# Optimization experiments

Hardware: AMD Instinct MI355X
Metric: run time of the kernel (lower is better)

The kernel has to match this reference:

```python
import jax, jax.numpy as jnp
import numpy as np

C = 19          # EEG channels
NP = C * C      # 361 channel pairs
D = 256         # UNIFIED_FEATURE_DIM
H = 8           # num_heads
HD = D // H     # head dim


def _build_mask():
    # rel[p, q] = True iff key-pair q shares a channel with query-pair p
    idx = np.arange(NP)
    ci, cj = idx // C, idx % C
    rel = ((ci[:, None] == ci[None, :]) | (ci[:, None] == cj[None, :]) |
           (cj[:, None] == ci[None, :]) | (cj[:, None] == cj[None, :]))
    return jnp.asarray(rel.reshape(C, C, NP))  # (channel_i, j, key_pair)

MASK = _build_mask()


def setup_inputs() -> dict:
    key = jax.random.key(0)
    ks = jax.random.split(key, 6)
    s = 0.05
    return {
        "x": jax.random.normal(ks[0], (32, NP, D), jnp.float32),
        # 19 stacked nn.MultiheadAttention modules: in_proj (3D, D) = [Wq; Wk; Wv]
        "w_in": jax.random.normal(ks[1], (C, 3 * D, D), jnp.float32) * s,
        "b_in": jnp.zeros((C, 3 * D), jnp.float32),
        "w_out": jax.random.normal(ks[2], (C, D, D), jnp.float32) * s,
        "b_out": jnp.zeros((C, D), jnp.float32),
        # fusion: nn.Linear(D, D)
        "w_fuse": jax.random.normal(ks[3], (D, D), jnp.float32) * s,
        "b_fuse": jnp.zeros((D,), jnp.float32),
    }


def reference(x, w_in, b_in, w_out, b_out, w_fuse, b_fuse):
    # x: (B, 361, D). Pair p=(i,j) at index i*19+j uses attention module i,
    # query = x[:, p], keys/values = pairs sharing channel i or j (mask).
    B = x.shape[0]
    wq, wk, wv = w_in[:, :D], w_in[:, D:2 * D], w_in[:, 2 * D:]
    bq, bk, bv = b_in[:, :D], b_in[:, D:2 * D], b_in[:, 2 * D:]

    # Per-channel K/V projections over all 361 pairs: (C, B, NP, D)
    K = jnp.einsum('bnd,ced->cbne', x, wk) + bk[:, None, None, :]
    V = jnp.einsum('bnd,ced->cbne', x, wv) + bv[:, None, None, :]
    # Queries grouped by first channel i: x reshaped to (B, C, C, D)
    xq = x.reshape(B, C, C, D)
    Q = jnp.einsum('bcjd,ced->cbje', xq, wq) + bq[:, None, None, :]  # (C,B,C,D)

    Qh = Q.reshape(C, B, C, H, HD)
    Kh = K.reshape(C, B, NP, H, HD)
    Vh = V.reshape(C, B, NP, H, HD)

    scale = 1.0 / jnp.sqrt(jnp.asarray(HD, x.dtype))
    scores = jnp.einsum('cbqhe,cbkhe->cbhqk', Qh, Kh) * scale  # (C,B,H,C,NP)
    scores = jnp.where(MASK[:, None, None, :, :], scores, -jnp.inf)
    attn = jax.nn.softmax(scores, axis=-1)

    out = jnp.einsum('cbhqk,cbkhe->cbqhe', attn, Vh).reshape(C, B, C, D)
    out = jnp.einsum('cbqd,ced->cbqe', out, w_out) + b_out[:, None, None, :]
    out = out.transpose(1, 0, 2, 3).reshape(B, NP, D)  # back to (B, 361, D)

    # fusion ('linear') + residual
    return out @ w_fuse.T + b_fuse + x
```

## Files before the change

### kernel.cpp

```cpp
#include <hip/hip_runtime.h>

#define CC 19
#define NPOS 361
#define NPAD 384
#define DIM 256
#define TKEY 32
#define NTILES 12

#define LDS_BYTES 33792

using bf16x8 = __attribute__((ext_vector_type(8))) short;
using f16x4  = __attribute__((ext_vector_type(4))) _Float16;
using floatx4 = __attribute__((ext_vector_type(4))) float;
using uintx2 = __attribute__((ext_vector_type(2))) unsigned int;

__device__ __forceinline__ unsigned short f2bf(float f) {
  unsigned u = __builtin_bit_cast(unsigned, f);
  u += 0x7fffu + ((u >> 16) & 1u);
  return (unsigned short)(u >> 16);
}

__device__ __forceinline__ f16x4 pack4h(float a, float b, float c2, float d) {
  const auto h01 = __builtin_amdgcn_cvt_pkrtz(a, b);
  const auto h23 = __builtin_amdgcn_cvt_pkrtz(c2, d);
  uintx2 uv = {__builtin_bit_cast(unsigned, h01), __builtin_bit_cast(unsigned, h23)};
  return __builtin_bit_cast(f16x4, uv);
}

__global__ void conv_all_kernel(const float* __restrict__ x,
                                const float* __restrict__ w_in,
                                const float* __restrict__ w_out,
                                const float* __restrict__ w_fuse,
                                unsigned short* __restrict__ ws) {
  const int j = blockIdx.x * 256 + threadIdx.x;
  float4 v = make_float4(0.f, 0.f, 0.f, 0.f);
  unsigned short* dst;
  if (j < 786432) {
    const int row = j >> 6;
    const int off = (j & 63) << 2;
    const int b = row / NPAD;
    const int r = row - b * NPAD;
    if (r < NPOS) v = *(const float4*)&x[(b * NPOS + r) * DIM + off];
    dst = &ws[row * DIM + off];
  } else if (j < 1720320) {
    const int k = j - 786432;
    v = *(const float4*)&w_in[k << 2];
    dst = &ws[3145728 + (k << 2)];
  } else if (j < 2031616) {
    const int k = j - 1720320;
    v = *(const float4*)&w_out[k << 2];
    dst = &ws[6881280 + (k << 2)];
  } else {
    const int k = j - 2031616;
    v = *(const float4*)&w_fuse[k << 2];
    dst = &ws[8126464 + (k << 2)];
  }
  ushort4 o;
  o.x = f2bf(v.x); o.y = f2bf(v.y); o.z = f2bf(v.z); o.w = f2bf(v.w);
  *(ushort4*)dst = o;
}

__launch_bounds__(512, 2)
__global__ void cgca_kernel(const float* __restrict__ xf,
                            const float* __restrict__ b_in,
                            const float* __restrict__ b_out,
                            const float* __restrict__ b_fuse,
                            const unsigned short* __restrict__ xbf,
                            const unsigned short* __restrict__ wibf,
                            const unsigned short* __restrict__ wobf,
                            const unsigned short* __restrict__ wfbf,
                            float* __restrict__ out) {
  const int bid = blockIdx.x;
  const int xcd = bid & 7;
  const int slot = bid >> 3;
  int c, b;
  if (slot < 64) {
    c = ((slot >> 5) << 3) + xcd;
    b = slot & 31;
  } else {
    const int widx = ((slot - 64) << 3) + xcd;
    c = 16 + (widx >> 5);
    b = widx & 31;
  }

  const int tid = threadIdx.x;
  const int w = tid >> 6;
  const int lane = tid & 63;
  const int quad = lane >> 4;
  const int l16 = lane & 15;
  const int eh = w * 32;

  extern __shared__ char smem[];
  unsigned short* bufx0 = (unsigned short*)(smem);
  unsigned short* bufx1 = (unsigned short*)(smem + 16896);
  float* sL = (float*)(smem + 16896);

  const float scale = 0.17677669529663687f;
  const floatx4 fzero = {0.f, 0.f, 0.f, 0.f};

  f16x4 qf[2][2];
  {
    bf16x8 wq[2][8];
#pragma unroll
    for (int m4 = 0; m4 < 2; ++m4)
#pragma unroll
      for (int k = 0; k < 8; ++k)
        wq[m4][k] = *(const bf16x8*)&wibf[(c * 768 + eh + m4 * 16 + l16) * DIM + k * 32 + quad * 8];
    float bq[2][4];
#pragma unroll
    for (int m4 = 0; m4 < 2; ++m4) {
      const float4 bv4 = *(const float4*)&b_in[c * 768 + eh + m4 * 16 + quad * 4];
      bq[m4][0] = bv4.x; bq[m4][1] = bv4.y; bq[m4][2] = bv4.z; bq[m4][3] = bv4.w;
    }
#pragma unroll
    for (int mt = 0; mt < 2; ++mt) {
      const int xrow = b * NPAD + c * CC + mt * 16 + l16;
      bf16x8 xq[8];
#pragma unroll
      for (int k = 0; k < 8; ++k)
        xq[k] = *(const bf16x8*)&xbf[xrow * DIM + k * 32 + quad * 8];
#pragma unroll
      for (int m4 = 0; m4 < 2; ++m4) {
        floatx4 acc = fzero;
#pragma unroll
        for (int k = 0; k < 8; ++k)
          acc = __builtin_amdgcn_mfma_f32_16x16x32_bf16(wq[m4][k], xq[k], acc, 0, 0, 0);
        qf[mt][m4] = pack4h((acc[0] + bq[m4][0]) * scale, (acc[1] + bq[m4][1]) * scale,
                            (acc[2] + bq[m4][2]) * scale, (acc[3] + bq[m4][3]) * scale);
      }
    }
  }

  bf16x8 wk[2][8], wv[2][8];
#pragma unroll
  for (int m4 = 0; m4 < 2; ++m4)
#pragma unroll
    for (int k = 0; k < 8; ++k) {
      wk[m4][k] =
          *(const bf16x8*)&wibf[(c * 768 + 256 + eh + m4 * 16 + l16) * DIM + k * 32 + quad * 8];
      wv[m4][k] =
          *(const bf16x8*)&wibf[(c * 768 + 512 + eh + m4 * 16 + l16) * DIM + k * 32 + quad * 8];
    }
  float bk[2][4];
#pragma unroll
  for (int m4 = 0; m4 < 2; ++m4) {
    const float4 bv4 = *(const float4*)&b_in[c * 768 + 256 + eh + m4 * 16 + quad * 4];
    bk[m4][0] = bv4.x; bk[m4][1] = bv4.y; bk[m4][2] = bv4.z; bk[m4][3] = bv4.w;
  }
  float bV[2];
#pragma unroll
  for (int ne = 0; ne < 2; ++ne) bV[ne] = b_in[c * 768 + 512 + eh + ne * 16 + l16];

#pragma unroll
  for (int it = 0; it < 2; ++it) {
    const int cc2 = tid + it * 512;
    const int row = cc2 >> 5;
    const int col = (cc2 & 31) * 8;
    *(bf16x8*)&bufx0[row * 264 + col] = *(const bf16x8*)&xbf[(b * NPAD + row) * DIM + col];
  }

  floatx4 o_acc[2][2];
  float lsum[2] = {0.f, 0.f};
#pragma unroll
  for (int mt = 0; mt < 2; ++mt)
#pragma unroll
    for (int ne = 0; ne < 2; ++ne) o_acc[mt][ne] = fzero;

  __syncthreads();

  for (int t = 0; t < NTILES; ++t) {
    const int t0 = t * TKEY;
    unsigned short* bx  = (t & 1) ? bufx1 : bufx0;
    unsigned short* bxn = (t & 1) ? bufx0 : bufx1;

    if (t + 1 < NTILES) {
#pragma unroll
      for (int it = 0; it < 2; ++it) {
        const int cc2 = tid + it * 512;
        const int row = cc2 >> 5;
        const int col = (cc2 & 31) * 8;
        *(bf16x8*)&bxn[row * 264 + col] =
            *(const bf16x8*)&xbf[(b * NPAD + t0 + TKEY + row) * DIM + col];
      }
    }

    floatx4 aK[2][2], aV[2][2];
#pragma unroll
    for (int i = 0; i < 2; ++i)
#pragma unroll
      for (int j = 0; j < 2; ++j) { aK[i][j] = fzero; aV[i][j] = fzero; }
#pragma unroll
    for (int k = 0; k < 8; ++k) {
      bf16x8 xfr[2];
#pragma unroll
      for (int n4 = 0; n4 < 2; ++n4)
        xfr[n4] = *(const bf16x8*)&bx[(n4 * 16 + l16) * 264 + k * 32 + quad * 8];
#pragma unroll
      for (int m4 = 0; m4 < 2; ++m4)
#pragma unroll
        for (int n4 = 0; n4 < 2; ++n4) {
          aK[m4][n4] = __builtin_amdgcn_mfma_f32_16x16x32_bf16(wk[m4][k], xfr[n4], aK[m4][n4], 0, 0, 0);
          aV[n4][m4] = __builtin_amdgcn_mfma_f32_16x16x32_bf16(xfr[n4], wv[m4][k], aV[n4][m4], 0, 0, 0);
        }
    }
    __syncthreads();

    f16x4 kf[2][2];
    f16x4 vf[2][2];
#pragma unroll
    for (int kt = 0; kt < 2; ++kt)
#pragma unroll
      for (int ec = 0; ec < 2; ++ec) {
        kf[kt][ec] = pack4h(aK[ec][kt][0] + bk[ec][0], aK[ec][kt][1] + bk[ec][1],
                            aK[ec][kt][2] + bk[ec][2], aK[ec][kt][3] + bk[ec][3]);
        vf[kt][ec] = pack4h(aV[kt][ec][0] + bV[ec], aV[kt][ec][1] + bV[ec],
                            aV[kt][ec][2] + bV[ec], aV[kt][ec][3] + bV[ec]);
      }

#pragma unroll
    for (int mt = 0; mt < 2; ++mt) {
      const unsigned q = (unsigned)(mt * 16 + l16);
      f16x4 pf[2];
#pragma unroll
      for (int kt = 0; kt < 2; ++kt) {
        floatx4 s = __builtin_amdgcn_mfma_f32_16x16x16f16(kf[kt][0], qf[mt][0], fzero, 0, 0, 0);
        s = __builtin_amdgcn_mfma_f32_16x16x16f16(kf[kt][1], qf[mt][1], s, 0, 0, 0);
        const int kbase = t0 + kt * 16 + quad * 4;
        float p[4];
#pragma unroll
        for (int r = 0; r < 4; ++r) {
          const int kabs = kbase + r;
          const unsigned ki = ((unsigned)kabs * 110377u) >> 21;
          const unsigned kj = (unsigned)kabs - ki * 19u;
          const bool ok = (kabs < NPOS) &&
                          (ki == (unsigned)c || kj == (unsigned)c || ki == q || kj == q);
          p[r] = ok ? __expf(s[r]) : 0.f;
        }
        lsum[mt] += (p[0] + p[1]) + (p[2] + p[3]);
        pf[kt] = pack4h(p[0], p[1], p[2], p[3]);
      }
#pragma unroll
      for (int kt = 0; kt < 2; ++kt)
#pragma unroll
        for (int ne = 0; ne < 2; ++ne)
          o_acc[mt][ne] =
              __builtin_amdgcn_mfma_f32_16x16x16f16(pf[kt], vf[kt][ne], o_acc[mt][ne], 0, 0, 0);
    }
  }

#pragma unroll
  for (int mt = 0; mt < 2; ++mt) {
    lsum[mt] += __shfl_xor(lsum[mt], 16);
    lsum[mt] += __shfl_xor(lsum[mt], 32);
  }
  if (lane < 16) {
    sL[w * 32 + lane] = lsum[0];
    sL[w * 32 + 16 + lane] = lsum[1];
  }
  float invl[2][4];
#pragma unroll
  for (int mt = 0; mt < 2; ++mt)
#pragma unroll
    for (int r = 0; r < 4; ++r)
      invl[mt][r] = 1.f / sL[w * 32 + mt * 16 + quad * 4 + r];

#pragma unroll
  for (int mt = 0; mt < 2; ++mt)
#pragma unroll
    for (int ne = 0; ne < 2; ++ne)
#pragma unroll
      for (int r = 0; r < 4; ++r)
        bufx0[(mt * 16 + quad * 4 + r) * 264 + eh + ne * 16 + l16] =
            f2bf(o_acc[mt][ne][r] * invl[mt][r]);
  __syncthreads();

#pragma unroll
  for (int mt = 0; mt < 2; ++mt) {
    bf16x8 a8[8];
#pragma unroll
    for (int k = 0; k < 8; ++k)
      a8[k] = *(const bf16x8*)&bufx0[(mt * 16 + l16) * 264 + k * 32 + quad * 8];
#pragma unroll
    for (int nt2 = 0; nt2 < 2; ++nt2) {
      const int e0 = w * 32 + nt2 * 16;
      floatx4 acc = fzero;
#pragma unroll
      for (int k = 0; k < 8; ++k) {
        bf16x8 b8 = *(const bf16x8*)&wobf[(c * 256 + e0 + l16) * DIM + k * 32 + quad * 8];
        acc = __builtin_amdgcn_mfma_f32_16x16x32_bf16(a8[k], b8, acc, 0, 0, 0);
      }
      const float bias = b_out[c * 256 + e0 + l16];
#pragma unroll
      for (int r = 0; r < 4; ++r)
        bufx1[(mt * 16 + quad * 4 + r) * 264 + e0 + l16] = f2bf(acc[r] + bias);
    }
  }
  __syncthreads();

#pragma unroll
  for (int mt = 0; mt < 2; ++mt) {
    bf16x8 a8[8];
#pragma unroll
    for (int k = 0; k < 8; ++k)
      a8[k] = *(const bf16x8*)&bufx1[(mt * 16 + l16) * 264 + k * 32 + quad * 8];
#pragma unroll
    for (int nt2 = 0; nt2 < 2; ++nt2) {
      const int e0 = w * 32 + nt2 * 16;
      floatx4 acc = fzero;
#pragma unroll
      for (int k = 0; k < 8; ++k) {
        bf16x8 b8 = *(const bf16x8*)&wfbf[(e0 + l16) * DIM + k * 32 + quad * 8];
        acc = __builtin_amdgcn_mfma_f32_16x16x32_bf16(a8[k], b8, acc, 0, 0, 0);
      }
      const float bfu = b_fuse[e0 + l16];
#pragma unroll
      for (int r = 0; r < 4; ++r) {
        const int row = mt * 16 + quad * 4 + r;
        if (row < CC) {
          const int gp = (b * NPOS + c * CC + row) * DIM + e0 + l16;
          out[gp] = acc[r] + bfu + xf[gp];
        }
      }
    }
  }
}

extern "C" void kernel_launch(void* const* d_in, const int* in_sizes, int n_in,
                              void* d_out, int out_size, void* d_ws, size_t ws_size,
                              hipStream_t stream) {
  const float* x      = (const float*)d_in[0];
  const float* w_in   = (const float*)d_in[1];
  const float* b_in   = (const float*)d_in[2];
  const float* w_out  = (const float*)d_in[3];
  const float* b_out  = (const float*)d_in[4];
  const float* w_fuse = (const float*)d_in[5];
  const float* b_fuse = (const float*)d_in[6];
  float* out = (float*)d_out;

  if (ws_size < (size_t)16384000) return;

  unsigned short* ws = (unsigned short*)d_ws;
  unsigned short* x_bf  = ws;
  unsigned short* wi_bf = ws + 3145728;
  unsigned short* wo_bf = ws + 6881280;
  unsigned short* wf_bf = ws + 8126464;

  conv_all_kernel<<<8000, 256, 0, stream>>>(x, w_in, w_out, w_fuse, ws);

  (void)hipFuncSetAttribute((const void*)cgca_kernel,
                            hipFuncAttributeMaxDynamicSharedMemorySize, LDS_BYTES);
  cgca_kernel<<<608, 512, LDS_BYTES, stream>>>(x, b_in, b_out, b_fuse, x_bf, wi_bf,
                                               wo_bf, wf_bf, out);
}
```

Before: 254.2 us.

## Quad-buffer key tiles, precompute attention mask bitmasks, fold scale into exp2

```diff
diff --git a/kernel.cpp b/kernel.cpp
--- a/kernel.cpp
+++ b/kernel.cpp
@@ -7,7 +7,7 @@
 #define TKEY 32
 #define NTILES 12
 
-#define LDS_BYTES 33792
+#define LDS_BYTES 70144
 
 using bf16x8 = __attribute__((ext_vector_type(8))) short;
 using f16x4  = __attribute__((ext_vector_type(4))) _Float16;
@@ -91,11 +91,13 @@
   const int eh = w * 32;
 
   extern __shared__ char smem[];
-  unsigned short* bufx0 = (unsigned short*)(smem);
-  unsigned short* bufx1 = (unsigned short*)(smem + 16896);
-  float* sL = (float*)(smem + 16896);
-
-  const float scale = 0.17677669529663687f;
+  unsigned short* sx = (unsigned short*)smem;
+  unsigned* msk = (unsigned*)(smem + 67584);
+  float* sL = (float*)(smem + 69120);
+  unsigned short* bufx0 = sx;
+  unsigned short* bufx1 = sx + 8448;
+
+  const float scale = 0.25503486f;
   const floatx4 fzero = {0.f, 0.f, 0.f, 0.f};
 
   f16x4 qf[2][2];
@@ -141,23 +143,37 @@
       wv[m4][k] =
           *(const bf16x8*)&wibf[(c * 768 + 512 + eh + m4 * 16 + l16) * DIM + k * 32 + quad * 8];
     }
-  float bk[2][4];
-#pragma unroll
-  for (int m4 = 0; m4 < 2; ++m4) {
-    const float4 bv4 = *(const float4*)&b_in[c * 768 + 256 + eh + m4 * 16 + quad * 4];
-    bk[m4][0] = bv4.x; bk[m4][1] = bv4.y; bk[m4][2] = bv4.z; bk[m4][3] = bv4.w;
-  }
   float bV[2];
 #pragma unroll
   for (int ne = 0; ne < 2; ++ne) bV[ne] = b_in[c * 768 + 512 + eh + ne * 16 + l16];
 
-#pragma unroll
-  for (int it = 0; it < 2; ++it) {
-    const int cc2 = tid + it * 512;
-    const int row = cc2 >> 5;
-    const int col = (cc2 & 31) * 8;
-    *(bf16x8*)&bufx0[row * 264 + col] = *(const bf16x8*)&xbf[(b * NPAD + row) * DIM + col];
-  }
+  {
+    const int q = tid >> 4;
+    const int wd = tid & 15;
+    if (wd < 12) {
+      unsigned m = 0u;
+      for (int i = 0; i < 32; ++i) {
+        const int kabs = wd * 32 + i;
+        const unsigned ki = ((unsigned)kabs * 110377u) >> 21;
+        const unsigned kj = (unsigned)kabs - ki * 19u;
+        if (kabs < NPOS && (ki == (unsigned)c || kj == (unsigned)c ||
+                            ki == (unsigned)q || kj == (unsigned)q))
+          m |= (1u << i);
+      }
+      msk[q * 12 + wd] = m;
+    }
+  }
+
+#pragma unroll
+  for (int u = 0; u < 2; ++u)
+#pragma unroll
+    for (int it = 0; it < 2; ++it) {
+      const int cc2 = tid + it * 512;
+      const int row = cc2 >> 5;
+      const int col = (cc2 & 31) * 8;
+      *(bf16x8*)&sx[u * 8448 + row * 264 + col] =
+          *(const bf16x8*)&xbf[(b * NPAD + u * TKEY + row) * DIM + col];
+    }
 
   floatx4 o_acc[2][2];
   float lsum[2] = {0.f, 0.f};
@@ -168,84 +184,87 @@
 
   __syncthreads();
 
-  for (int t = 0; t < NTILES; ++t) {
-    const int t0 = t * TKEY;
-    unsigned short* bx  = (t & 1) ? bufx1 : bufx0;
-    unsigned short* bxn = (t & 1) ? bufx0 : bufx1;
-
-    if (t + 1 < NTILES) {
-#pragma unroll
-      for (int it = 0; it < 2; ++it) {
-        const int cc2 = tid + it * 512;
-        const int row = cc2 >> 5;
-        const int col = (cc2 & 31) * 8;
-        *(bf16x8*)&bxn[row * 264 + col] =
-            *(const bf16x8*)&xbf[(b * NPAD + t0 + TKEY + row) * DIM + col];
-      }
-    }
-
-    floatx4 aK[2][2], aV[2][2];
-#pragma unroll
-    for (int i = 0; i < 2; ++i)
-#pragma unroll
-      for (int j = 0; j < 2; ++j) { aK[i][j] = fzero; aV[i][j] = fzero; }
-#pragma unroll
-    for (int k = 0; k < 8; ++k) {
-      bf16x8 xfr[2];
-#pragma unroll
-      for (int n4 = 0; n4 < 2; ++n4)
-        xfr[n4] = *(const bf16x8*)&bx[(n4 * 16 + l16) * 264 + k * 32 + quad * 8];
-#pragma unroll
-      for (int m4 = 0; m4 < 2; ++m4)
-#pragma unroll
-        for (int n4 = 0; n4 < 2; ++n4) {
-          aK[m4][n4] = __builtin_amdgcn_mfma_f32_16x16x32_bf16(wk[m4][k], xfr[n4], aK[m4][n4], 0, 0, 0);
-          aV[n4][m4] = __builtin_amdgcn_mfma_f32_16x16x32_bf16(xfr[n4], wv[m4][k], aV[n4][m4], 0, 0, 0);
+  for (int s6 = 0; s6 < 6; ++s6) {
+    const int tb = s6 * 2;
+    if (s6 < 5) {
+#pragma unroll
+      for (int u = 0; u < 2; ++u) {
+        const int t = tb + 2 + u;
+        unsigned short* bxn = sx + (t & 3) * 8448;
+#pragma unroll
+        for (int it = 0; it < 2; ++it) {
+          const int cc2 = tid + it * 512;
+          const int row = cc2 >> 5;
+          const int col = (cc2 & 31) * 8;
+          *(bf16x8*)&bxn[row * 264 + col] =
+              *(const bf16x8*)&xbf[(b * NPAD + t * TKEY + row) * DIM + col];
         }
+      }
+    }
+
+#pragma unroll
+    for (int u = 0; u < 2; ++u) {
+      const int t = tb + u;
+      const int t0 = t * TKEY;
+      const unsigned short* bx = sx + (t & 3) * 8448;
+
+      floatx4 aK[2][2], aV[2][2];
+#pragma unroll
+      for (int i = 0; i < 2; ++i)
+#pragma unroll
+        for (int j = 0; j < 2; ++j) { aK[i][j] = fzero; aV[i][j] = fzero; }
+#pragma unroll
+      for (int k = 0; k < 8; ++k) {
+        bf16x8 xfr[2];
+#pragma unroll
+        for (int n4 = 0; n4 < 2; ++n4)
+          xfr[n4] = *(const bf16x8*)&bx[(n4 * 16 + l16) * 264 + k * 32 + quad * 8];
+#pragma unroll
+        for (int m4 = 0; m4 < 2; ++m4)
+#pragma unroll
+          for (int n4 = 0; n4 < 2; ++n4) {
+            aK[m4][n4] = __builtin_amdgcn_mfma_f32_16x16x32_bf16(wk[m4][k], xfr[n4], aK[m4][n4], 0, 0, 0);
+            aV[n4][m4] = __builtin_amdgcn_mfma_f32_16x16x32_bf16(xfr[n4], wv[m4][k], aV[n4][m4], 0, 0, 0);
+          }
+      }
+
+      f16x4 kf[2][2];
+      f16x4 vf[2][2];
+#pragma unroll
+      for (int kt = 0; kt < 2; ++kt)
+#pragma unroll
+        for (int ec = 0; ec < 2; ++ec) {
+          kf[kt][ec] = pack4h(aK[ec][kt][0], aK[ec][kt][1], aK[ec][kt][2], aK[ec][kt][3]);
+          vf[kt][ec] = pack4h(aV[kt][ec][0], aV[kt][ec][1], aV[kt][ec][2], aV[kt][ec][3]);
+        }
+
+#pragma unroll
+      for (int mt = 0; mt < 2; ++mt) {
+        const int q = mt * 16 + l16;
+        const unsigned mw = msk[q * 12 + t];
+        f16x4 pf[2];
+#pragma unroll
+        for (int kt = 0; kt < 2; ++kt) {
+          floatx4 s2 = __builtin_amdgcn_mfma_f32_16x16x16f16(kf[kt][0], qf[mt][0], fzero, 0, 0, 0);
+          s2 = __builtin_amdgcn_mfma_f32_16x16x16f16(kf[kt][1], qf[mt][1], s2, 0, 0, 0);
+          const unsigned mk = mw >> (kt * 16 + quad * 4);
+          float p[4];
+#pragma unroll
+          for (int r = 0; r < 4; ++r)
+            p[r] = (mk & (1u << r)) ? __builtin_exp2f(s2[r]) : 0.f;
+          lsum[mt] += (p[0] + p[1]) + (p[2] + p[3]);
+          pf[kt] = pack4h(p[0], p[1], p[2], p[3]);
+        }
+#pragma unroll
+        for (int kt = 0; kt < 2; ++kt)
+#pragma unroll
+          for (int ne = 0; ne < 2; ++ne)
+            o_acc[mt][ne] =
+                __builtin_amdgcn_mfma_f32_16x16x16f16(pf[kt], vf[kt][ne], o_acc[mt][ne], 0, 0, 0);
+      }
+      (void)t0;
     }
     __syncthreads();
-
-    f16x4 kf[2][2];
-    f16x4 vf[2][2];
-#pragma unroll
-    for (int kt = 0; kt < 2; ++kt)
-#pragma unroll
-      for (int ec = 0; ec < 2; ++ec) {
-        kf[kt][ec] = pack4h(aK[ec][kt][0] + bk[ec][0], aK[ec][kt][1] + bk[ec][1],
-                            aK[ec][kt][2] + bk[ec][2], aK[ec][kt][3] + bk[ec][3]);
-        vf[kt][ec] = pack4h(aV[kt][ec][0] + bV[ec], aV[kt][ec][1] + bV[ec],
-                            aV[kt][ec][2] + bV[ec], aV[kt][ec][3] + bV[ec]);
-      }
-
-#pragma unroll
-    for (int mt = 0; mt < 2; ++mt) {
-      const unsigned q = (unsigned)(mt * 16 + l16);
-      f16x4 pf[2];
-#pragma unroll
-      for (int kt = 0; kt < 2; ++kt) {
-        floatx4 s = __builtin_amdgcn_mfma_f32_16x16x16f16(kf[kt][0], qf[mt][0], fzero, 0, 0, 0);
-        s = __builtin_amdgcn_mfma_f32_16x16x16f16(kf[kt][1], qf[mt][1], s, 0, 0, 0);
-        const int kbase = t0 + kt * 16 + quad * 4;
-        float p[4];
-#pragma unroll
-        for (int r = 0; r < 4; ++r) {
-          const int kabs = kbase + r;
-          const unsigned ki = ((unsigned)kabs * 110377u) >> 21;
-          const unsigned kj = (unsigned)kabs - ki * 19u;
-          const bool ok = (kabs < NPOS) &&
-                          (ki == (unsigned)c || kj == (unsigned)c || ki == q || kj == q);
-          p[r] = ok ? __expf(s[r]) : 0.f;
-        }
-        lsum[mt] += (p[0] + p[1]) + (p[2] + p[3]);
-        pf[kt] = pack4h(p[0], p[1], p[2], p[3]);
-      }
-#pragma unroll
-      for (int kt = 0; kt < 2; ++kt)
-#pragma unroll
-        for (int ne = 0; ne < 2; ++ne)
-          o_acc[mt][ne] =
-              __builtin_amdgcn_mfma_f32_16x16x16f16(pf[kt], vf[kt][ne], o_acc[mt][ne], 0, 0, 0);
-    }
   }
 
 #pragma unroll
@@ -271,7 +290,7 @@
 #pragma unroll
       for (int r = 0; r < 4; ++r)
         bufx0[(mt * 16 + quad * 4 + r) * 264 + eh + ne * 16 + l16] =
-            f2bf(o_acc[mt][ne][r] * invl[mt][r]);
+            f2bf(o_acc[mt][ne][r] * invl[mt][r] + bV[ne]);
   __syncthreads();
 
 #pragma unroll
```

Result: faster. 249.1 us (-2.0%).
